# Kernel tuning notes

Hardware: AMD Instinct MI355X
Metric: run time of the kernel (lower is better)

Reference implementation:

```python
import jax, jax.numpy as jnp
import numpy as np

B, S, D, H = 4, 2048, 1024, 16
d = D // H
SCALE = d ** -0.5


def setup_inputs() -> dict:
    key = jax.random.key(0)
    k1, k2, k3 = jax.random.split(key, 3)
    x = jax.random.normal(k1, (B, S, D), dtype=jnp.float32)
    # causal keep-mask (True = keep), shape (B, 1, S, S)
    causal = jnp.tril(jnp.ones((S, S), dtype=bool))
    mask = jnp.broadcast_to(causal[None, None, :, :], (B, 1, S, S))
    # nn.Linear(D, 3D, bias=False): weight (3D, D); out_proj weight (D, D)
    w_qkv = jax.random.normal(k2, (3 * D, D), dtype=jnp.float32) * (D ** -0.5)
    w_out = jax.random.normal(k3, (D, D), dtype=jnp.float32) * (D ** -0.5)
    return {"x": x, "mask": mask, "w_qkv": w_qkv, "w_out": w_out}


def reference(x, mask, w_qkv, w_out):
    # qkv projection: y = x @ W^T, split into q, k, v
    qkv = jnp.einsum('bsd,ed->bse', x, w_qkv)  # (B, S, 3D)
    q, k, v = jnp.split(qkv, 3, axis=-1)
    # (B, S, H, d) -> (B, H, S, d)
    q = q.reshape(B, S, H, d).transpose(0, 2, 1, 3)
    k = k.reshape(B, S, H, d).transpose(0, 2, 1, 3)
    v = v.reshape(B, S, H, d).transpose(0, 2, 1, 3)
    # scores (B, H, S, S)
    attn = jnp.einsum('bhqd,bhkd->bhqk', q, k) * SCALE
    attn = jnp.where(mask, attn, -jnp.inf)
    attn = jax.nn.softmax(attn, axis=-1)
    out = jnp.einsum('bhqk,bhkd->bhqd', attn, v)
    out = out.transpose(0, 2, 1, 3).reshape(B, S, D)
    out = jnp.einsum('bsd,ed->bse', out, w_out)
    return out, (k, v)
```

## Files before the change

kernel.cpp:

```cpp
#include <hip/hip_runtime.h>
#include <hip/hip_bf16.h>

typedef __bf16 bf16_t;
typedef bf16_t bf16x8 __attribute__((ext_vector_type(8)));
typedef bf16_t bf16x4 __attribute__((ext_vector_type(4)));
typedef float  f32x4  __attribute__((ext_vector_type(4)));
typedef float  f32x8  __attribute__((ext_vector_type(8)));
typedef float  f32x16 __attribute__((ext_vector_type(16)));

#define B_  4
#define S_  2048
#define D_  1024
#define H_  16
#define HD  64

#define QSCALE 0.1803368801111204f

#define KV_TILE_ELEMS 4096
#define KV_BH_ELEMS   262144

__device__ __forceinline__ void async_copy16(const void* g, void* l) {
    __builtin_amdgcn_global_load_lds((const __attribute__((address_space(1))) void*)g,
                                     (__attribute__((address_space(3))) void*)l,
                                     16, 0, 0);
}

__device__ __forceinline__ float fast_exp2(float x) {
    float r;
    asm("v_exp_f32 %0, %1" : "=v"(r) : "v"(x));
    return r;
}

__global__ __launch_bounds__(256) void cvt_kernel(const float* __restrict__ in,
                                                  bf16_t* __restrict__ out, int n4) {
    int i = blockIdx.x * 256 + threadIdx.x;
    if (i >= n4) return;
    float4 f = ((const float4*)in)[i];
    bf16x4 o = { (bf16_t)f.x, (bf16_t)f.y, (bf16_t)f.z, (bf16_t)f.w };
    ((bf16x4*)out)[i] = o;
}

__device__ __forceinline__ void gemm_tile(const bf16_t* __restrict__ A,
                                          const bf16_t* __restrict__ Bt,
                                          int lda, int ldb, int m0, int n0, int K,
                                          bf16_t* As, bf16_t* Bs, f32x4 acc[4][4]) {
    const int lane = threadIdx.x & 63;
    const int wv   = threadIdx.x >> 6;
    const int wm   = wv >> 1, wn = wv & 1;
    const int r8   = lane >> 3, c8 = lane & 7;
    const int lo   = lane & 15, hi = lane >> 4;

    for (int k0 = 0; k0 < K; k0 += 64) {
        #pragma unroll
        for (int i = 0; i < 4; ++i) {
            const int c   = wv * 4 + i;
            const int row = c * 8 + r8;
            async_copy16(A  + (size_t)(m0 + row) * lda + k0 + c8 * 8, As + c * 512);
            async_copy16(Bt + (size_t)(n0 + row) * ldb + k0 + c8 * 8, Bs + c * 512);
        }
        __syncthreads();
        #pragma unroll
        for (int kk = 0; kk < 2; ++kk) {
            const int ko = kk * 32 + hi * 8;
            bf16x8 aF[4], bF[4];
            #pragma unroll
            for (int m = 0; m < 4; ++m)
                aF[m] = *(const bf16x8*)(As + (wm * 64 + m * 16 + lo) * 64 + ko);
            #pragma unroll
            for (int n = 0; n < 4; ++n)
                bF[n] = *(const bf16x8*)(Bs + (wn * 64 + n * 16 + lo) * 64 + ko);
            #pragma unroll
            for (int m = 0; m < 4; ++m)
                #pragma unroll
                for (int n = 0; n < 4; ++n)
                    acc[m][n] = __builtin_amdgcn_mfma_f32_16x16x32_bf16(aF[m], bF[n], acc[m][n], 0, 0, 0);
        }
        __syncthreads();
    }
}

__global__ __launch_bounds__(256) void gemm_qkv_kernel(const bf16_t* __restrict__ A,
                                                       const bf16_t* __restrict__ Bt,
                                                       float* __restrict__ out,
                                                       bf16_t* __restrict__ q_ws,
                                                       bf16_t* __restrict__ kv_frag) {
    __shared__ __align__(16) bf16_t As[128 * 64];
    __shared__ __align__(16) bf16_t Bs[128 * 64];
    const int m0 = blockIdx.y * 128, n0 = blockIdx.x * 128;
    const f32x4 zero = {0.f, 0.f, 0.f, 0.f};
    f32x4 acc[4][4];
    #pragma unroll
    for (int m = 0; m < 4; ++m)
        #pragma unroll
        for (int n = 0; n < 4; ++n) acc[m][n] = zero;

    gemm_tile(A, Bt, D_, D_, m0, n0, D_, As, Bs, acc);

    const int lane = threadIdx.x & 63, wv = threadIdx.x >> 6;
    const int wm = wv >> 1, wn = wv & 1;
    const int lo = lane & 15, hi = lane >> 4;
    #pragma unroll
    for (int m = 0; m < 4; ++m) {
        #pragma unroll
        for (int n = 0; n < 4; ++n) {
            const int gcol = n0 + wn * 64 + n * 16 + lo;
            const int sec  = gcol >> 10;
            const int e    = gcol & 1023;
            const int h    = e >> 6, dv = e & 63;
            #pragma unroll
            for (int j4 = 0; j4 < 4; ++j4) {
                const int grow = m0 + wm * 64 + m * 16 + hi * 4 + j4;
                const float v  = acc[m][n][j4];
                const int b = grow >> 11, s = grow & 2047;
                const size_t idx = ((((size_t)b * H_ + h) * S_ + s) << 6) + dv;
                if (sec == 0) {
                    q_ws[idx] = (bf16_t)(v * QSCALE);
                } else if (sec == 1) {
                    out[8388608u + idx] = v;
                    const int bh   = b * H_ + h;
                    const int tile = s >> 5, ql = s & 31;
                    const int c    = dv >> 4, hb = (dv >> 3) & 1, jj = dv & 7;
                    kv_frag[(((size_t)bh * 64 + tile) * 8 + c) * 512 + hb * 256 + ql * 8 + jj] = (bf16_t)v;
                } else {
                    out[16777216u + idx] = v;
                }
            }
        }
    }
}

__global__ __launch_bounds__(256) void build_vfrag_kernel(const float* __restrict__ v_f32,
                                                          bf16_t* __restrict__ kv_frag) {
    __shared__ __align__(16) bf16_t T[64][72];
    const int bh = blockIdx.x;
    const int s0 = blockIdx.y * 64;
    const int t  = threadIdx.x;
    {
        const int sl  = t >> 2;
        const int dv0 = (t & 3) * 16;
        const float* src = v_f32 + ((size_t)bh * S_ + s0 + sl) * HD + dv0;
        float tmp[16];
        #pragma unroll
        for (int i = 0; i < 4; ++i) *(float4*)(tmp + i * 4) = ((const float4*)src)[i];
        #pragma unroll
        for (int i = 0; i < 16; ++i) T[dv0 + i][sl] = (bf16_t)tmp[i];
    }
    __syncthreads();
    {
        const int st = t >> 7;
        const int r  = t & 127;
        const int cc = r >> 5;
        const int l  = r & 31;
        const int khi = cc >> 1, hd = cc & 1;
        const int d   = hd * 32 + l;
        const int tile = (s0 >> 5) + st;
        bf16_t* dst = kv_frag + (((size_t)bh * 64 + tile) * 8 + 4 + cc) * 512 + l * 8;
        const int slb = st * 32 + khi * 16;
        *(bf16x8*)(dst)       = *(const bf16x8*)&T[d][slb];
        *(bf16x8*)(dst + 256) = *(const bf16x8*)&T[d][slb + 8];
    }
}

__global__ __launch_bounds__(256) void attn_kernel(const bf16_t* __restrict__ q_ws,
                                                   const bf16_t* __restrict__ kv_frag,
                                                   bf16_t* __restrict__ attn_ws) {
    __shared__ __align__(16) float MRG[2][2][64][20];
    __shared__ float LSUM[2][64];
    __shared__ __align__(16) bf16_t T[2][32][72];
    const int lane = threadIdx.x & 63;
    const int wv   = threadIdx.x >> 6;
    const int blk   = blockIdx.x;
    const int x     = blk & 7;
    const int r     = blk >> 3;
    const int bh    = x + 8 * (r & 7);
    const int pr    = wv >> 1;
    const int khalf = wv & 1;
    const int p     = (r >> 3) * 2 + pr;

    const int ql = lane & 31;
    const int hb = lane >> 5;
    const size_t kv_base = (size_t)bh * (S_ * HD);
    const int b = bh >> 4, h = bh & 15;

    const bf16_t* kvb = kv_frag + (size_t)bh * KV_BH_ELEMS + (size_t)lane * 8;

    auto load_k = [&](int tile, bf16x8 kf[4]) {
        const bf16_t* tp = kvb + (size_t)tile * KV_TILE_ELEMS;
        #pragma unroll
        for (int c = 0; c < 4; ++c) kf[c] = *(const bf16x8*)(tp + c * 512);
    };
    auto load_v = [&](int tile, bf16x8 vf[4]) {
        const bf16_t* tp = kvb + (size_t)tile * KV_TILE_ELEMS + 2048;
        #pragma unroll
        for (int i = 0; i < 4; ++i) vf[i] = *(const bf16x8*)(tp + i * 512);
    };

    #pragma unroll 1
    for (int pass = 0; pass < 2; ++pass) {
        const int qblock = pass ? (63 - p) : p;
        const int q0 = qblock * 32;
        const int nt  = qblock + 1;
        const int mid = nt >> 1;
        const int tstart = khalf ? mid : 0;
        const int tend   = khalf ? nt  : mid;

        bf16x8 qF[4];
        const bf16_t* qrow = q_ws + kv_base + (size_t)(q0 + ql) * HD + hb * 8;
        #pragma unroll
        for (int c = 0; c < 4; ++c) qF[c] = *(const bf16x8*)(qrow + 16 * c);

        f32x16 accT0 = {}, accT1 = {};
        float lsum = 0.f;

        auto compute_tile = [&](const bf16x8 kf[4], const bf16x8 vf[4], bool diag) {
            f32x16 s = {};
            #pragma unroll
            for (int c = 0; c < 4; ++c)
                s = __builtin_amdgcn_mfma_f32_32x32x16_bf16(kf[c], qF[c], s, 0, 0, 0);
            if (diag) {
                #pragma unroll
                for (int rr = 0; rr < 16; ++rr) {
                    const int kloc = (rr & 3) + 8 * (rr >> 2) + 4 * hb;
                    if (kloc > ql) s[rr] = -1e30f;
                }
            }
            #pragma unroll
            for (int rr = 0; rr < 16; ++rr) s[rr] = fast_exp2(s[rr]);
            f32x8 t8 = __builtin_shufflevector(s, s, 0, 1, 2, 3, 4, 5, 6, 7) +
                       __builtin_shufflevector(s, s, 8, 9, 10, 11, 12, 13, 14, 15);
            f32x4 t4 = __builtin_shufflevector(t8, t8, 0, 1, 2, 3) +
                       __builtin_shufflevector(t8, t8, 4, 5, 6, 7);
            lsum += (t4[0] + t4[1]) + (t4[2] + t4[3]);

            unsigned w[8];
            #pragma unroll
            for (int i = 0; i < 8; ++i) {
                unsigned d;
                asm("v_cvt_pk_bf16_f32 %0, %1, %2" : "=v"(d) : "v"(s[2 * i]), "v"(s[2 * i + 1]));
                w[i] = d;
            }
            union { unsigned u[4]; bf16x8 v; } pf0, pf1;
            {
                auto r0 = __builtin_amdgcn_permlane32_swap(w[0], w[2], false, false);
                auto r1 = __builtin_amdgcn_permlane32_swap(w[1], w[3], false, false);
                pf0.u[0] = r0[0]; pf0.u[1] = r1[0]; pf0.u[2] = r0[1]; pf0.u[3] = r1[1];
            }
            {
                auto r0 = __builtin_amdgcn_permlane32_swap(w[4], w[6], false, false);
                auto r1 = __builtin_amdgcn_permlane32_swap(w[5], w[7], false, false);
                pf1.u[0] = r0[0]; pf1.u[1] = r1[0]; pf1.u[2] = r0[1]; pf1.u[3] = r1[1];
            }

            accT0 = __builtin_amdgcn_mfma_f32_32x32x16_bf16(vf[0], pf0.v, accT0, 0, 0, 0);
            accT1 = __builtin_amdgcn_mfma_f32_32x32x16_bf16(vf[1], pf0.v, accT1, 0, 0, 0);
            accT0 = __builtin_amdgcn_mfma_f32_32x32x16_bf16(vf[2], pf1.v, accT0, 0, 0, 0);
            accT1 = __builtin_amdgcn_mfma_f32_32x32x16_bf16(vf[3], pf1.v, accT1, 0, 0, 0);
        };

        int t = tstart;
        for (; t + 1 < tend; t += 2) {
            bf16x8 kA[4], vA[4], kB[4], vB[4];
            load_k(t, kA);
            load_v(t, vA);
            load_k(t + 1, kB);
            load_v(t + 1, vB);
            compute_tile(kA, vA, t == qblock);
            compute_tile(kB, vB, (t + 1) == qblock);
        }
        if (t < tend) {
            bf16x8 kA[4], vA[4];
            load_k(t, kA);
            load_v(t, vA);
            compute_tile(kA, vA, t == qblock);
        }

        if (khalf) {
            *(f32x16*)&MRG[pr][0][lane][0] = accT0;
            *(f32x16*)&MRG[pr][1][lane][0] = accT1;
            LSUM[pr][lane] = lsum;
        }
        __syncthreads();
        if (!khalf) {
            accT0 += *(const f32x16*)&MRG[pr][0][lane][0];
            accT1 += *(const f32x16*)&MRG[pr][1][lane][0];
            lsum  += LSUM[pr][lane];
            const float ltot = lsum + __shfl_xor(lsum, 32, 64);
            const float inv  = 1.0f / ltot;
            #pragma unroll
            for (int rr = 0; rr < 16; ++rr) {
                const int dl = (rr & 3) + 8 * (rr >> 2) + 4 * hb;
                T[pr][ql][dl]      = (bf16_t)(accT0[rr] * inv);
                T[pr][ql][32 + dl] = (bf16_t)(accT1[rr] * inv);
            }
            asm volatile("s_waitcnt lgkmcnt(0)" ::: "memory");
            #pragma unroll
            for (int it = 0; it < 4; ++it) {
                const int ch  = it * 64 + lane;
                const int row = ch >> 3, c8 = ch & 7;
                bf16x8 o = *(const bf16x8*)&T[pr][row][c8 * 8];
                *(bf16x8*)(attn_ws + ((size_t)(b * S_ + q0 + row)) * D_ + h * HD + c8 * 8) = o;
            }
        }
        __syncthreads();
    }
}

__global__ __launch_bounds__(256) void gemm_out_kernel(const bf16_t* __restrict__ A,
                                                       const bf16_t* __restrict__ Bt,
                                                       float* __restrict__ out) {
    __shared__ __align__(16) bf16_t As[128 * 64];
    __shared__ __align__(16) bf16_t Bs[128 * 64];
    const int m0 = blockIdx.y * 128, n0 = blockIdx.x * 128;
    const f32x4 zero = {0.f, 0.f, 0.f, 0.f};
    f32x4 acc[4][4];
    #pragma unroll
    for (int m = 0; m < 4; ++m)
        #pragma unroll
        for (int n = 0; n < 4; ++n) acc[m][n] = zero;

    gemm_tile(A, Bt, D_, D_, m0, n0, D_, As, Bs, acc);

    const int lane = threadIdx.x & 63, wv = threadIdx.x >> 6;
    const int wm = wv >> 1, wn = wv & 1;
    const int lo = lane & 15, hi = lane >> 4;
    #pragma unroll
    for (int m = 0; m < 4; ++m) {
        #pragma unroll
        for (int n = 0; n < 4; ++n) {
            const int gcol = n0 + wn * 64 + n * 16 + lo;
            #pragma unroll
            for (int j = 0; j < 4; ++j) {
                const int grow = m0 + wm * 64 + m * 16 + hi * 4 + j;
                out[(size_t)grow * D_ + gcol] = acc[m][n][j];
            }
        }
    }
}

extern "C" void kernel_launch(void* const* d_in, const int* in_sizes, int n_in,
                              void* d_out, int out_size, void* d_ws, size_t ws_size,
                              hipStream_t stream) {
    (void)in_sizes; (void)n_in; (void)out_size; (void)ws_size;
    const float* x     = (const float*)d_in[0];
    const float* w_qkv = (const float*)d_in[2];
    const float* w_out = (const float*)d_in[3];
    float* out = (float*)d_out;
    char* ws = (char*)d_ws;

    bf16_t* x_bf    = (bf16_t*)(ws);
    bf16_t* wqkv_bf = (bf16_t*)(ws + 16777216);
    bf16_t* wout_bf = (bf16_t*)(ws + 23068672);
    bf16_t* q_ws    = (bf16_t*)(ws + 25165824);
    bf16_t* kv_frag = (bf16_t*)(ws + 41943040);
    bf16_t* attn_ws = (bf16_t*)(ws + 75497472);

    cvt_kernel<<<8192, 256, 0, stream>>>(x, x_bf, 2097152);
    cvt_kernel<<<3072, 256, 0, stream>>>(w_qkv, wqkv_bf, 786432);
    cvt_kernel<<<1024, 256, 0, stream>>>(w_out, wout_bf, 262144);

    gemm_qkv_kernel<<<dim3(24, 64), 256, 0, stream>>>(x_bf, wqkv_bf, out, q_ws, kv_frag);
    build_vfrag_kernel<<<dim3(64, 32), 256, 0, stream>>>(out + 16777216, kv_frag);
    attn_kernel<<<1024, 256, 0, stream>>>(q_ws, kv_frag, attn_ws);
    gemm_out_kernel<<<dim3(8, 64), 256, 0, stream>>>(attn_ws, wout_bf, out);
}
```

Measured before the change: 196.4 us.

## Fuse V fragment build into QKV GEMM epilogue and remap blocks per XCD

The separate build_vfrag kernel is removed, and the QKV GEMM epilogue now writes V directly into the bf16 fragment layout used by attention. This saves one launch and a full re-read of fp32 V. Both GEMMs also switch to a 1D grid that groups N-tiles per XCD (bid&7), so blocks sharing a weight slice land on the same L2. The cost is that the epilogue writes V fragments as scattered 2-byte stores instead of the coalesced transposed writes the old kernel made.

```diff
diff --git a/kernel.cpp b/kernel.cpp
--- a/kernel.cpp
+++ b/kernel.cpp
@@ -86,7 +86,11 @@
                                                        bf16_t* __restrict__ kv_frag) {
     __shared__ __align__(16) bf16_t As[128 * 64];
     __shared__ __align__(16) bf16_t Bs[128 * 64];
-    const int m0 = blockIdx.y * 128, n0 = blockIdx.x * 128;
+    const int bid = blockIdx.x;
+    const int xcd = bid & 7, idx = bid >> 3;
+    const int n_t = xcd * 3 + (idx % 3);
+    const int m_t = idx / 3;
+    const int m0 = m_t * 128, n0 = n_t * 128;
     const f32x4 zero = {0.f, 0.f, 0.f, 0.f};
     f32x4 acc[4][4];
     #pragma unroll
@@ -112,52 +116,24 @@
                 const int grow = m0 + wm * 64 + m * 16 + hi * 4 + j4;
                 const float v  = acc[m][n][j4];
                 const int b = grow >> 11, s = grow & 2047;
-                const size_t idx = ((((size_t)b * H_ + h) * S_ + s) << 6) + dv;
+                const size_t idx2 = ((((size_t)b * H_ + h) * S_ + s) << 6) + dv;
+                const int bh   = b * H_ + h;
+                const int tile = s >> 5;
                 if (sec == 0) {
-                    q_ws[idx] = (bf16_t)(v * QSCALE);
+                    q_ws[idx2] = (bf16_t)(v * QSCALE);
                 } else if (sec == 1) {
-                    out[8388608u + idx] = v;
-                    const int bh   = b * H_ + h;
-                    const int tile = s >> 5, ql = s & 31;
-                    const int c    = dv >> 4, hb = (dv >> 3) & 1, jj = dv & 7;
+                    out[8388608u + idx2] = v;
+                    const int ql = s & 31;
+                    const int c  = dv >> 4, hb = (dv >> 3) & 1, jj = dv & 7;
                     kv_frag[(((size_t)bh * 64 + tile) * 8 + c) * 512 + hb * 256 + ql * 8 + jj] = (bf16_t)v;
                 } else {
-                    out[16777216u + idx] = v;
+                    out[16777216u + idx2] = v;
+                    const int khi = (s >> 4) & 1, hb = (s >> 3) & 1, jj = s & 7;
+                    const int hd  = dv >> 5, l = dv & 31;
+                    kv_frag[(((size_t)bh * 64 + tile) * 8 + 4 + khi * 2 + hd) * 512 + hb * 256 + l * 8 + jj] = (bf16_t)v;
                 }
             }
         }
-    }
-}
-
-__global__ __launch_bounds__(256) void build_vfrag_kernel(const float* __restrict__ v_f32,
-                                                          bf16_t* __restrict__ kv_frag) {
-    __shared__ __align__(16) bf16_t T[64][72];
-    const int bh = blockIdx.x;
-    const int s0 = blockIdx.y * 64;
-    const int t  = threadIdx.x;
-    {
-        const int sl  = t >> 2;
-        const int dv0 = (t & 3) * 16;
-        const float* src = v_f32 + ((size_t)bh * S_ + s0 + sl) * HD + dv0;
-        float tmp[16];
-        #pragma unroll
-        for (int i = 0; i < 4; ++i) *(float4*)(tmp + i * 4) = ((const float4*)src)[i];
-        #pragma unroll
-        for (int i = 0; i < 16; ++i) T[dv0 + i][sl] = (bf16_t)tmp[i];
-    }
-    __syncthreads();
-    {
-        const int st = t >> 7;
-        const int r  = t & 127;
-        const int cc = r >> 5;
-        const int l  = r & 31;
-        const int khi = cc >> 1, hd = cc & 1;
-        const int d   = hd * 32 + l;
-        const int tile = (s0 >> 5) + st;
-        bf16_t* dst = kv_frag + (((size_t)bh * 64 + tile) * 8 + 4 + cc) * 512 + l * 8;
-        const int slb = st * 32 + khi * 16;
-        *(bf16x8*)(dst)       = *(const bf16x8*)&T[d][slb];
-        *(bf16x8*)(dst + 256) = *(const bf16x8*)&T[d][slb + 8];
     }
 }
 
@@ -310,7 +286,9 @@
                                                        float* __restrict__ out) {
     __shared__ __align__(16) bf16_t As[128 * 64];
     __shared__ __align__(16) bf16_t Bs[128 * 64];
-    const int m0 = blockIdx.y * 128, n0 = blockIdx.x * 128;
+    const int bid = blockIdx.x;
+    const int xcd = bid & 7, idx = bid >> 3;
+    const int m0 = idx * 128, n0 = xcd * 128;
     const f32x4 zero = {0.f, 0.f, 0.f, 0.f};
     f32x4 acc[4][4];
     #pragma unroll
@@ -358,8 +336,7 @@
     cvt_kernel<<<3072, 256, 0, stream>>>(w_qkv, wqkv_bf, 786432);
     cvt_kernel<<<1024, 256, 0, stream>>>(w_out, wout_bf, 262144);
 
-    gemm_qkv_kernel<<<dim3(24, 64), 256, 0, stream>>>(x_bf, wqkv_bf, out, q_ws, kv_frag);
-    build_vfrag_kernel<<<dim3(64, 32), 256, 0, stream>>>(out + 16777216, kv_frag);
+    gemm_qkv_kernel<<<1536, 256, 0, stream>>>(x_bf, wqkv_bf, out, q_ws, kv_frag);
     attn_kernel<<<1024, 256, 0, stream>>>(q_ws, kv_frag, attn_ws);
-    gemm_out_kernel<<<dim3(8, 64), 256, 0, stream>>>(attn_ws, wout_bf, out);
-}
+    gemm_out_kernel<<<512, 256, 0, stream>>>(attn_ws, wout_bf, out);
+}
```

After: 196.0 us. Within noise of the previous version (-0.2%).
